# Kernel tuning notes

Measured on AMD Instinct MI355X. Metric: run time of the kernel, lower is better.

The kernel has to match this reference:

```python
import jax, jax.numpy as jnp
import numpy as np

B, N, D = 2, 2048, 256
H, HID, EN = 8, 64, 2
ALPHA = 0.2
NEG = -9e15


def setup_inputs() -> dict:
    key = jax.random.key(0)
    k1, k2, k3, k4, k5, k6 = jax.random.split(key, 6)
    fea_mats = jax.random.normal(k1, (B, N, D), dtype=jnp.float32)
    adj_mats = jax.random.randint(k2, (B, N, N), 0, 2).astype(jnp.float32)
    # xavier-uniform-like init (gain 1.414)
    def xav(k, shape):
        fan_in, fan_out = shape[-2], shape[-1]
        bound = 1.414 * np.sqrt(6.0 / (fan_in + fan_out))
        return jax.random.uniform(k, shape, jnp.float32, -bound, bound)
    W_att = xav(k3, (H, D, HID))          # per-head projection
    a_att = xav(k4, (H, 2 * HID, 1))      # per-head attention vector
    W_last = xav(k5, (H * HID, EN))       # last-layer projection
    a_last = xav(k6, (2 * EN, 1))         # last-layer attention vector
    return {"fea_mats": fea_mats, "adj_mats": adj_mats,
            "W_att": W_att, "a_att": a_att,
            "W_last": W_last, "a_last": a_last}


def _leaky(x):
    return jnp.where(x >= 0, x, ALPHA * x)


def _masked_attn(e, adj):
    # torch: where(adj!=0, e, 0) * adj; masked_fill(==0, -9e15); softmax(dim=1 over columns)
    att = jnp.where(adj != 0, e, jnp.zeros_like(e)) * adj
    att = jnp.where(att == 0, jnp.full_like(att, NEG), att)
    return jax.nn.softmax(att, axis=-1)


def reference(fea_mats, adj_mats, W_att, a_att, W_last, a_last):
    # ---- multi-head GAT layers (concat=True), eval mode -> dropout = identity ----
    wh = jnp.einsum('bnd,hdo->bhno', fea_mats, W_att)        # [B,H,N,HID]
    a1 = a_att[:, :HID, 0]                                   # [H,HID]
    a2 = a_att[:, HID:, 0]                                   # [H,HID]
    e1 = jnp.einsum('bhno,ho->bhn', wh, a1)                  # regulon part
    e2 = jnp.einsum('bhno,ho->bhn', wh, a2)                  # gene part
    e = _leaky(e1[:, :, :, None] + e2[:, :, None, :])        # [B,H,N,N]
    att = _masked_attn(e, adj_mats[:, None])                 # [B,H,N,N]
    x = jax.nn.elu(jnp.einsum('bhnm,bhmo->bhno', att, wh))   # [B,H,N,HID]
    x = jnp.transpose(x, (0, 2, 1, 3)).reshape(B, N, H * HID)
    # ---- last layer (concat=False), adj narrowed to square (already square) ----
    wh2 = jnp.einsum('bnd,de->bne', x, W_last)               # [B,N,EN]
    b1 = a_last[:EN, 0]
    b2 = a_last[EN:, 0]
    e = _leaky(jnp.einsum('bne,e->bn', wh2, b1)[:, :, None]
               + jnp.einsum('bne,e->bn', wh2, b2)[:, None, :])  # [B,N,N]
    att = _masked_attn(e, adj_mats)
    out = jax.nn.elu(jnp.einsum('bnm,bme->bne', att, wh2))   # [B,N,EN]
    return out
```

## Files before the change

kernel.cpp:

```cpp
#include <hip/hip_runtime.h>
#include <hip/hip_bf16.h>
#include <cstdint>
#include <cstddef>

#define B_ 2
#define N_ 2048
#define D_ 256
#define H_ 8
#define HID_ 64
#define EN_ 2
#define ALPHA 0.2f
#define NEGBIG (-3.0e38f)
#define LOG2E 1.4426950408889634f

typedef __bf16 bf16x8 __attribute__((ext_vector_type(8)));
typedef float f32x4 __attribute__((ext_vector_type(4)));
typedef unsigned short ushort8 __attribute__((ext_vector_type(8)));
typedef float float4v __attribute__((ext_vector_type(4)));
typedef float float2v __attribute__((ext_vector_type(2)));

__device__ __forceinline__ unsigned short f2bf(float f) {
    unsigned int u = __builtin_bit_cast(unsigned int, f);
    unsigned int r = u + 0x7FFFu + ((u >> 16) & 1u);
    return (unsigned short)(r >> 16);
}
__device__ __forceinline__ float leakyf(float x) { return fmaxf(x, ALPHA * x); }

__device__ __forceinline__ ushort8 cvt8(const float* __restrict__ p) {
    float4v x0 = *(const float4v*)p;
    float4v x1 = *(const float4v*)(p + 4);
    ushort8 r;
    #pragma unroll
    for (int e = 0; e < 4; ++e) { r[e] = f2bf(x0[e]); r[e + 4] = f2bf(x1[e]); }
    return r;
}

__global__ void k_transpose_w(const float* __restrict__ W,
                              unsigned short* __restrict__ WT) {
    int h = blockIdx.x;
    const float* Wh = W + (size_t)h * D_ * HID_;
    unsigned short* WTh = WT + (size_t)h * HID_ * D_;
    for (int idx = threadIdx.x; idx < D_ * HID_; idx += blockDim.x) {
        int d = idx / HID_, o = idx % HID_;
        WTh[o * D_ + d] = f2bf(Wh[idx]);
    }
}

__global__ __launch_bounds__(256) void k_wh(
    const float* __restrict__ fea,
    const unsigned short* __restrict__ WT,
    const float* __restrict__ a_att,
    unsigned short* __restrict__ whT,
    float* __restrict__ e1, float* __restrict__ e2)
{
    int bid = blockIdx.x;
    int i0 = (bid & 31) << 6;
    int h  = (bid >> 5) & 7;
    int b  = bid >> 8;

    __shared__ __align__(16) union SmemA {
        struct { unsigned short fa[64 * 72]; unsigned short wt[64 * 72]; } s;
        float tr[64 * 65];
    } u;

    int t = threadIdx.x;
    int lane = t & 63;
    int wv = t >> 6;
    int r = lane & 15, q = lane >> 4;
    int ra = t >> 2;
    int cc = (t & 3) * 16;

    f32x4 acc[4] = {};

    const float* fearow = fea + ((size_t)(b * N_ + i0 + ra)) * D_;
    const unsigned short* wtrow = WT + ((size_t)(h * 64 + ra)) * D_;

    for (int d0 = 0; d0 < D_; d0 += 64) {
        *(ushort8*)&u.s.fa[ra * 72 + cc]     = cvt8(fearow + d0 + cc);
        *(ushort8*)&u.s.fa[ra * 72 + cc + 8] = cvt8(fearow + d0 + cc + 8);
        *(ushort8*)&u.s.wt[ra * 72 + cc]     = *(const ushort8*)(wtrow + d0 + cc);
        *(ushort8*)&u.s.wt[ra * 72 + cc + 8] = *(const ushort8*)(wtrow + d0 + cc + 8);
        __syncthreads();
        #pragma unroll
        for (int k0 = 0; k0 < 64; k0 += 32) {
            bf16x8 a = *(const bf16x8*)&u.s.fa[(16 * wv + r) * 72 + k0 + q * 8];
            #pragma unroll
            for (int f = 0; f < 4; ++f) {
                bf16x8 bb = *(const bf16x8*)&u.s.wt[(16 * f + r) * 72 + k0 + q * 8];
                acc[f] = __builtin_amdgcn_mfma_f32_16x16x32_bf16(a, bb, acc[f], 0, 0, 0);
            }
        }
        __syncthreads();
    }

    float a1v[4], a2v[4];
    #pragma unroll
    for (int f = 0; f < 4; ++f) {
        a1v[f] = a_att[h * 128 + 16 * f + r];
        a2v[f] = a_att[h * 128 + 64 + 16 * f + r];
    }
    #pragma unroll
    for (int rr = 0; rr < 4; ++rr) {
        float s1 = 0.f, s2 = 0.f;
        #pragma unroll
        for (int f = 0; f < 4; ++f) { s1 += acc[f][rr] * a1v[f]; s2 += acc[f][rr] * a2v[f]; }
        #pragma unroll
        for (int m = 1; m < 16; m <<= 1) {
            s1 += __shfl_xor(s1, m, 64);
            s2 += __shfl_xor(s2, m, 64);
        }
        if (r == 0) {
            int i = i0 + 16 * wv + 4 * q + rr;
            size_t idx = ((size_t)(b * H_ + h)) * N_ + i;
            e1[idx] = s1 * LOG2E; e2[idx] = s2 * LOG2E;
        }
    }

    #pragma unroll
    for (int f = 0; f < 4; ++f)
        #pragma unroll
        for (int rr = 0; rr < 4; ++rr)
            u.tr[(16 * f + r) * 65 + 16 * wv + 4 * q + rr] = acc[f][rr];
    __syncthreads();
    {
        int o = t >> 2;
        int ch = (t & 3) * 16;
        unsigned short tmp[16];
        #pragma unroll
        for (int e = 0; e < 16; ++e) tmp[e] = f2bf(u.tr[o * 65 + ch + e]);
        ushort8* dst = (ushort8*)(whT + (((size_t)(b * H_ + h) * 64 + o)) * N_ + i0 + ch);
        dst[0] = *(ushort8*)&tmp[0];
        dst[1] = *(ushort8*)&tmp[8];
    }
}

__global__ __launch_bounds__(256) void k_maxe2(const float* __restrict__ e2,
                                               float* __restrict__ mx) {
    int bh = blockIdx.x;
    int t = threadIdx.x;
    const float* row = e2 + (size_t)bh * N_;
    float M = NEGBIG;
    #pragma unroll
    for (int it = 0; it < N_ / 256; ++it) M = fmaxf(M, row[it * 256 + t]);
    #pragma unroll
    for (int s = 1; s < 64; s <<= 1) M = fmaxf(M, __shfl_xor(M, s, 64));
    __shared__ float red[4];
    if ((t & 63) == 0) red[t >> 6] = M;
    __syncthreads();
    if (t == 0) mx[bh] = fmaxf(fmaxf(red[0], red[1]), fmaxf(red[2], red[3]));
}

template<int JPER>
__global__ __launch_bounds__(256) void k_pv1(
    const float* __restrict__ adj,
    const unsigned short* __restrict__ whT,
    const float* __restrict__ e1, const float* __restrict__ e2,
    const float* __restrict__ maxE2,
    float* __restrict__ x_part,
    float* __restrict__ zPart)
{
    constexpr int NT = JPER / 64;
    int s  = blockIdx.x;
    int i0 = blockIdx.y << 6;
    int bh = blockIdx.z;
    int h = bh & 7, b = bh >> 3;
    int jBeg = s * JPER;

    __shared__ __align__(16) unsigned short p_lds[64 * 72];
    __shared__ __align__(16) unsigned short wt_lds[64 * 72];

    int t = threadIdx.x;
    int lane = t & 63;
    int wv = t >> 6;
    int r = lane & 15, q = lane >> 4;
    int ra = t >> 2;
    int cc = (t & 3) * 16;

    size_t rowIdx = ((size_t)bh) * N_ + i0 + ra;
    float eRow = e1[rowIdx];
    float m = leakyf(eRow + maxE2[bh]);
    float eRm = eRow - m;
    float eR2 = ALPHA * eRow - m;
    const float* e2row = e2 + ((size_t)bh) * N_;
    const float* abase = adj + ((size_t)(b * N_ + i0 + ra)) * N_ + jBeg + cc;
    const unsigned short* wbase = whT + (((size_t)bh) * 64 + ra) * N_ + jBeg + cc;

    bf16x8 ones;
    #pragma unroll
    for (int e = 0; e < 8; ++e) ones[e] = (__bf16)1.0f;

    f32x4 acc[4] = {};
    f32x4 accz = {};

    float4v avN[4];
    #pragma unroll
    for (int u4 = 0; u4 < 4; ++u4) avN[u4] = *(const float4v*)(abase + u4 * 4);

    #pragma unroll 1
    for (int t8 = 0; t8 < NT; ++t8) {
        float4v ev[4];
        #pragma unroll
        for (int u4 = 0; u4 < 4; ++u4)
            ev[u4] = *(const float4v*)(e2row + jBeg + t8 * 64 + cc + u4 * 4);

        float pf[16];
        #pragma unroll
        for (int e = 0; e < 16; ++e) {
            float e2v = ev[e >> 2][e & 3];
            float t0 = eRm + e2v;
            float t1 = __builtin_fmaf(ALPHA, e2v, eR2);
            float p = __builtin_amdgcn_exp2f(fmaxf(t0, t1));
            pf[e] = p * avN[e >> 2][e & 3];
        }
        if (t8 + 1 < NT) {
            #pragma unroll
            for (int u4 = 0; u4 < 4; ++u4)
                avN[u4] = *(const float4v*)(abase + (t8 + 1) * 64 + u4 * 4);
        }
        bf16x8 pv0, pv1;
        #pragma unroll
        for (int e = 0; e < 8; ++e) { pv0[e] = (__bf16)pf[e]; pv1[e] = (__bf16)pf[e + 8]; }
        *(bf16x8*)&p_lds[ra * 72 + cc]     = pv0;
        *(bf16x8*)&p_lds[ra * 72 + cc + 8] = pv1;
        *(ushort8*)&wt_lds[ra * 72 + cc]     = *(const ushort8*)(wbase + t8 * 64);
        *(ushort8*)&wt_lds[ra * 72 + cc + 8] = *(const ushort8*)(wbase + t8 * 64 + 8);
        __syncthreads();
        #pragma unroll
        for (int k0 = 0; k0 < 64; k0 += 32) {
            bf16x8 a = *(const bf16x8*)&p_lds[(16 * wv + r) * 72 + k0 + q * 8];
            accz = __builtin_amdgcn_mfma_f32_16x16x32_bf16(a, ones, accz, 0, 0, 0);
            #pragma unroll
            for (int f = 0; f < 4; ++f) {
                bf16x8 bb = *(const bf16x8*)&wt_lds[(16 * f + r) * 72 + k0 + q * 8];
                acc[f] = __builtin_amdgcn_mfma_f32_16x16x32_bf16(a, bb, acc[f], 0, 0, 0);
            }
        }
        __syncthreads();
    }

    float* xp = x_part + (size_t)s * (B_ * N_) * 512;
    #pragma unroll
    for (int f = 0; f < 4; ++f) {
        #pragma unroll
        for (int rr = 0; rr < 4; ++rr) {
            int i = i0 + 16 * wv + 4 * q + rr;
            xp[((size_t)(b * N_ + i)) * 512 + h * 64 + 16 * f + r] = acc[f][rr];
        }
    }
    if (r == 0) {
        #pragma unroll
        for (int rr = 0; rr < 4; ++rr) {
            int i = i0 + 16 * wv + 4 * q + rr;
            zPart[((size_t)(s * 16 + bh)) * N_ + i] = accz[rr];
        }
    }
}

__global__ __launch_bounds__(256) void k_wh2(
    const float* __restrict__ x_part,
    const float* __restrict__ zPart,
    const float* __restrict__ W_last,
    const float* __restrict__ a_last,
    float* __restrict__ wh2, float* __restrict__ g1, float* __restrict__ g2,
    int S)
{
    int idx = blockIdx.x * 4 + (threadIdx.x >> 6);
    int lane = threadIdx.x & 63;
    int b = idx >> 11, n = idx & (N_ - 1);
    float a0 = 0.f, a1 = 0.f;
    #pragma unroll
    for (int it = 0; it < 8; ++it) {
        int k = it * 64 + lane;
        float xv = 0.f, zv = 0.f;
        for (int s = 0; s < S; ++s) {
            xv += x_part[((size_t)s * (B_ * N_) + idx) * 512 + k];
            zv += zPart[((size_t)(s * 16 + b * 8 + it)) * N_ + n];
        }
        float x = (zv > 0.f) ? xv / zv : 0.f;
        x = x > 0.f ? x : expm1f(x);
        float2v wl = *(const float2v*)(W_last + k * 2);
        a0 += x * wl[0];
        a1 += x * wl[1];
    }
    #pragma unroll
    for (int s = 1; s < 64; s <<= 1) {
        a0 += __shfl_xor(a0, s, 64);
        a1 += __shfl_xor(a1, s, 64);
    }
    if (lane == 0) {
        wh2[idx * 2] = a0; wh2[idx * 2 + 1] = a1;
        g1[idx] = (a0 * a_last[0] + a1 * a_last[1]) * LOG2E;
        g2[idx] = (a0 * a_last[2] + a1 * a_last[3]) * LOG2E;
    }
}

__global__ __launch_bounds__(256) void k_out(
    const float* __restrict__ adj,
    const float* __restrict__ wh2,
    const float* __restrict__ g1, const float* __restrict__ g2,
    float* __restrict__ out)
{
    int idx = blockIdx.x * 4 + (threadIdx.x >> 6);
    int lane = threadIdx.x & 63;
    int b = idx >> 11;
    float gi = g1[idx];
    const float* arow = adj + (size_t)idx * N_;
    const float* g2b = g2 + (size_t)b * N_;
    const float* wh2b = wh2 + (size_t)b * N_ * 2;

    float ep[32];
    float M = NEGBIG;
    #pragma unroll
    for (int it = 0; it < 8; ++it) {
        int j = it * 256 + lane * 4;
        float4v a4 = *(const float4v*)(arow + j);
        float4v s4 = *(const float4v*)(g2b + j);
        #pragma unroll
        for (int e = 0; e < 4; ++e) {
            float l = leakyf(gi + s4[e]);
            float v = (a4[e] != 0.f) ? l : NEGBIG;
            ep[it * 4 + e] = v;
            M = fmaxf(M, v);
        }
    }
    #pragma unroll
    for (int s = 1; s < 64; s <<= 1) M = fmaxf(M, __shfl_xor(M, s, 64));

    float Z = 0.f, A0 = 0.f, A1 = 0.f;
    #pragma unroll
    for (int it = 0; it < 8; ++it) {
        int j = it * 256 + lane * 4;
        float4v wA = *(const float4v*)(wh2b + 2 * j);
        float4v wB = *(const float4v*)(wh2b + 2 * j + 4);
        #pragma unroll
        for (int e = 0; e < 4; ++e) {
            float p = __builtin_amdgcn_exp2f(ep[it * 4 + e] - M);
            Z += p;
            float w0 = (e < 2) ? wA[2 * e] : wB[2 * (e - 2)];
            float w1 = (e < 2) ? wA[2 * e + 1] : wB[2 * (e - 2) + 1];
            A0 += p * w0;
            A1 += p * w1;
        }
    }
    #pragma unroll
    for (int s = 1; s < 64; s <<= 1) {
        Z += __shfl_xor(Z, s, 64);
        A0 += __shfl_xor(A0, s, 64);
        A1 += __shfl_xor(A1, s, 64);
    }
    if (lane == 0) {
        float o0 = A0 / Z, o1 = A1 / Z;
        o0 = o0 > 0.f ? o0 : expm1f(o0);
        o1 = o1 > 0.f ? o1 : expm1f(o1);
        float2v ov; ov[0] = o0; ov[1] = o1;
        *(float2v*)(out + idx * 2) = ov;
    }
}

extern "C" void kernel_launch(void* const* d_in, const int* in_sizes, int n_in,
                              void* d_out, int out_size, void* d_ws, size_t ws_size,
                              hipStream_t stream) {
    const float* fea    = (const float*)d_in[0];
    const float* adj    = (const float*)d_in[1];
    const float* W_att  = (const float*)d_in[2];
    const float* a_att  = (const float*)d_in[3];
    const float* W_last = (const float*)d_in[4];
    const float* a_last = (const float*)d_in[5];

    char* ws = (char*)d_ws;
    float* e1  = (float*)(ws + 0);
    float* e2  = (float*)(ws + 131072);
    float* mxE = (float*)(ws + 262144);
    float* wh2 = (float*)(ws + 262400);
    float* g1  = (float*)(ws + 295168);
    float* g2  = (float*)(ws + 311552);
    unsigned short* WT  = (unsigned short*)(ws + 327936);
    unsigned short* whT = (unsigned short*)(ws + 590080);
    float* zPart = (float*)(ws + 4784384);
    float* x_part = (float*)(ws + 5308672);

    const size_t BASE = 5308672ULL, XPART = 8388608ULL;
    int S = (ws_size >= BASE + 4 * XPART) ? 4
          : (ws_size >= BASE + 2 * XPART) ? 2 : 1;

    k_transpose_w<<<dim3(H_), dim3(256), 0, stream>>>(W_att, WT);
    k_wh<<<dim3(B_ * H_ * (N_ / 64)), dim3(256), 0, stream>>>(
        fea, WT, a_att, whT, e1, e2);
    k_maxe2<<<dim3(B_ * H_), dim3(256), 0, stream>>>(e2, mxE);
    if (S == 4)
        k_pv1<512><<<dim3(4, N_ / 64, B_ * H_), dim3(256), 0, stream>>>(
            adj, whT, e1, e2, mxE, x_part, zPart);
    else if (S == 2)
        k_pv1<1024><<<dim3(2, N_ / 64, B_ * H_), dim3(256), 0, stream>>>(
            adj, whT, e1, e2, mxE, x_part, zPart);
    else
        k_pv1<2048><<<dim3(1, N_ / 64, B_ * H_), dim3(256), 0, stream>>>(
            adj, whT, e1, e2, mxE, x_part, zPart);
    k_wh2<<<dim3(B_ * N_ / 4), dim3(256), 0, stream>>>(
        x_part, zPart, W_last, a_last, wh2, g1, g2, S);
    k_out<<<dim3(B_ * N_ / 4), dim3(256), 0, stream>>>(
        adj, wh2, g1, g2, (float*)d_out);
}
```

Before: 104.6 us.

## Compute attention probabilities directly in MFMA register layout, enlarge row tile

The main GAT attention-times-values kernel now builds the bf16 probability fragments in each lane's registers, already in MFMA A-operand order. This removes the P staging through LDS and one round of shared-memory writes and reads. Blocks grow to 512 threads covering 128 rows, so each wh^T tile loaded into LDS is shared by twice as many rows. The wh^T tile uses an XOR swizzle to avoid bank conflicts, and the adjacency prefetch across iterations is dropped, which may expose more global-load latency.

```diff
diff --git a/kernel.cpp b/kernel.cpp
--- a/kernel.cpp
+++ b/kernel.cpp
@@ -151,39 +151,43 @@
 }
 
 template<int JPER>
-__global__ __launch_bounds__(256) void k_pv1(
+__global__ __launch_bounds__(512, 4) void k_pv1(
     const float* __restrict__ adj,
     const unsigned short* __restrict__ whT,
-    const float* __restrict__ e1, const float* __restrict__ e2,
+    const float* __restrict__ e1g, const float* __restrict__ e2g,
     const float* __restrict__ maxE2,
     float* __restrict__ x_part,
     float* __restrict__ zPart)
 {
     constexpr int NT = JPER / 64;
     int s  = blockIdx.x;
-    int i0 = blockIdx.y << 6;
+    int i0 = blockIdx.y << 7;
     int bh = blockIdx.z;
     int h = bh & 7, b = bh >> 3;
     int jBeg = s * JPER;
 
-    __shared__ __align__(16) unsigned short p_lds[64 * 72];
-    __shared__ __align__(16) unsigned short wt_lds[64 * 72];
+    __shared__ __align__(16) unsigned short wt_lds[64 * 64];
 
     int t = threadIdx.x;
     int lane = t & 63;
     int wv = t >> 6;
     int r = lane & 15, q = lane >> 4;
-    int ra = t >> 2;
-    int cc = (t & 3) * 16;
-
-    size_t rowIdx = ((size_t)bh) * N_ + i0 + ra;
-    float eRow = e1[rowIdx];
+
+    int ir = i0 + 16 * wv + r;
+    float eRow = e1g[(size_t)bh * N_ + ir];
     float m = leakyf(eRow + maxE2[bh]);
     float eRm = eRow - m;
     float eR2 = ALPHA * eRow - m;
-    const float* e2row = e2 + ((size_t)bh) * N_;
-    const float* abase = adj + ((size_t)(b * N_ + i0 + ra)) * N_ + jBeg + cc;
-    const unsigned short* wbase = whT + (((size_t)bh) * 64 + ra) * N_ + jBeg + cc;
+
+    const float* e2p = e2g + (size_t)bh * N_ + jBeg;
+    const float* ap  = adj + ((size_t)(b * N_ + ir)) * N_ + jBeg;
+    const unsigned short* wsrc =
+        whT + ((size_t)bh * 64 + (t >> 3)) * N_ + jBeg + (t & 7) * 8;
+    unsigned short* wdst = &wt_lds[(t * 8) ^ (((t >> 3) & 7) << 3)];
+
+    int swz = (r & 7) << 3;
+    int koff0 = (8 * q) ^ swz;
+    int koff1 = (32 + 8 * q) ^ swz;
 
     bf16x8 ones;
     #pragma unroll
@@ -192,59 +196,60 @@
     f32x4 acc[4] = {};
     f32x4 accz = {};
 
-    float4v avN[4];
-    #pragma unroll
-    for (int u4 = 0; u4 < 4; ++u4) avN[u4] = *(const float4v*)(abase + u4 * 4);
-
     #pragma unroll 1
     for (int t8 = 0; t8 < NT; ++t8) {
-        float4v ev[4];
-        #pragma unroll
-        for (int u4 = 0; u4 < 4; ++u4)
-            ev[u4] = *(const float4v*)(e2row + jBeg + t8 * 64 + cc + u4 * 4);
-
-        float pf[16];
-        #pragma unroll
-        for (int e = 0; e < 16; ++e) {
-            float e2v = ev[e >> 2][e & 3];
-            float t0 = eRm + e2v;
-            float t1 = __builtin_fmaf(ALPHA, e2v, eR2);
-            float p = __builtin_amdgcn_exp2f(fmaxf(t0, t1));
-            pf[e] = p * avN[e >> 2][e & 3];
-        }
-        if (t8 + 1 < NT) {
-            #pragma unroll
-            for (int u4 = 0; u4 < 4; ++u4)
-                avN[u4] = *(const float4v*)(abase + (t8 + 1) * 64 + u4 * 4);
-        }
-        bf16x8 pv0, pv1;
-        #pragma unroll
-        for (int e = 0; e < 8; ++e) { pv0[e] = (__bf16)pf[e]; pv1[e] = (__bf16)pf[e + 8]; }
-        *(bf16x8*)&p_lds[ra * 72 + cc]     = pv0;
-        *(bf16x8*)&p_lds[ra * 72 + cc + 8] = pv1;
-        *(ushort8*)&wt_lds[ra * 72 + cc]     = *(const ushort8*)(wbase + t8 * 64);
-        *(ushort8*)&wt_lds[ra * 72 + cc + 8] = *(const ushort8*)(wbase + t8 * 64 + 8);
+        *(ushort8*)wdst = *(const ushort8*)(wsrc + t8 * 64);
+
+        const float* aj = ap + t8 * 64 + q * 8;
+        const float* ej = e2p + t8 * 64 + q * 8;
+        float4v a0 = *(const float4v*)(aj);
+        float4v a1 = *(const float4v*)(aj + 4);
+        float4v b0 = *(const float4v*)(aj + 32);
+        float4v b1 = *(const float4v*)(aj + 36);
+        float4v f0 = *(const float4v*)(ej);
+        float4v f1 = *(const float4v*)(ej + 4);
+        float4v g0 = *(const float4v*)(ej + 32);
+        float4v g1 = *(const float4v*)(ej + 36);
+        bf16x8 pa0, pa1;
+        #pragma unroll
+        for (int e = 0; e < 4; ++e) {
+            float p;
+            p = __builtin_amdgcn_exp2f(fmaxf(eRm + f0[e], __builtin_fmaf(ALPHA, f0[e], eR2)));
+            pa0[e] = (__bf16)(p * a0[e]);
+            p = __builtin_amdgcn_exp2f(fmaxf(eRm + f1[e], __builtin_fmaf(ALPHA, f1[e], eR2)));
+            pa0[e + 4] = (__bf16)(p * a1[e]);
+            p = __builtin_amdgcn_exp2f(fmaxf(eRm + g0[e], __builtin_fmaf(ALPHA, g0[e], eR2)));
+            pa1[e] = (__bf16)(p * b0[e]);
+            p = __builtin_amdgcn_exp2f(fmaxf(eRm + g1[e], __builtin_fmaf(ALPHA, g1[e], eR2)));
+            pa1[e + 4] = (__bf16)(p * b1[e]);
+        }
+
         __syncthreads();
-        #pragma unroll
-        for (int k0 = 0; k0 < 64; k0 += 32) {
-            bf16x8 a = *(const bf16x8*)&p_lds[(16 * wv + r) * 72 + k0 + q * 8];
-            accz = __builtin_amdgcn_mfma_f32_16x16x32_bf16(a, ones, accz, 0, 0, 0);
+        {
+            bf16x8 bb;
             #pragma unroll
             for (int f = 0; f < 4; ++f) {
-                bf16x8 bb = *(const bf16x8*)&wt_lds[(16 * f + r) * 72 + k0 + q * 8];
-                acc[f] = __builtin_amdgcn_mfma_f32_16x16x32_bf16(a, bb, acc[f], 0, 0, 0);
+                bb = *(const bf16x8*)&wt_lds[f * 1024 + r * 64 + koff0];
+                acc[f] = __builtin_amdgcn_mfma_f32_16x16x32_bf16(pa0, bb, acc[f], 0, 0, 0);
             }
+            accz = __builtin_amdgcn_mfma_f32_16x16x32_bf16(pa0, ones, accz, 0, 0, 0);
+            #pragma unroll
+            for (int f = 0; f < 4; ++f) {
+                bb = *(const bf16x8*)&wt_lds[f * 1024 + r * 64 + koff1];
+                acc[f] = __builtin_amdgcn_mfma_f32_16x16x32_bf16(pa1, bb, acc[f], 0, 0, 0);
+            }
+            accz = __builtin_amdgcn_mfma_f32_16x16x32_bf16(pa1, ones, accz, 0, 0, 0);
         }
         __syncthreads();
     }
 
-    float* xp = x_part + (size_t)s * (B_ * N_) * 512;
+    float* xp = x_part + ((size_t)s * (B_ * N_) + (size_t)b * N_) * 512 + h * 64;
     #pragma unroll
     for (int f = 0; f < 4; ++f) {
         #pragma unroll
         for (int rr = 0; rr < 4; ++rr) {
             int i = i0 + 16 * wv + 4 * q + rr;
-            xp[((size_t)(b * N_ + i)) * 512 + h * 64 + 16 * f + r] = acc[f][rr];
+            xp[(size_t)i * 512 + 16 * f + r] = acc[f][rr];
         }
     }
     if (r == 0) {
@@ -388,13 +393,13 @@
         fea, WT, a_att, whT, e1, e2);
     k_maxe2<<<dim3(B_ * H_), dim3(256), 0, stream>>>(e2, mxE);
     if (S == 4)
-        k_pv1<512><<<dim3(4, N_ / 64, B_ * H_), dim3(256), 0, stream>>>(
+        k_pv1<512><<<dim3(4, N_ / 128, B_ * H_), dim3(512), 0, stream>>>(
             adj, whT, e1, e2, mxE, x_part, zPart);
     else if (S == 2)
-        k_pv1<1024><<<dim3(2, N_ / 64, B_ * H_), dim3(256), 0, stream>>>(
+        k_pv1<1024><<<dim3(2, N_ / 128, B_ * H_), dim3(512), 0, stream>>>(
             adj, whT, e1, e2, mxE, x_part, zPart);
     else
-        k_pv1<2048><<<dim3(1, N_ / 64, B_ * H_), dim3(256), 0, stream>>>(
+        k_pv1<2048><<<dim3(1, N_ / 128, B_ * H_), dim3(512), 0, stream>>>(
             adj, whT, e1, e2, mxE, x_part, zPart);
     k_wh2<<<dim3(B_ * N_ / 4), dim3(256), 0, stream>>>(
         x_part, zPart, W_last, a_last, wh2, g1, g2, S);
```

After: 104.4 us. No clear change (-0.3%).
